# Performance work log

Hardware: AMD Instinct MI355X
Metric: run time of the kernel (lower is better)

The kernel has to match this reference:

```python
import jax, jax.numpy as jnp
import numpy as np

B, S, D = 512, 199, 128
PRO, SKILL = 20000, 500


def setup_inputs() -> dict:
    key = jax.random.key(0)
    ks = jax.random.split(key, 32)
    rn = lambda k, shape: jax.random.normal(k, shape, dtype=jnp.float32) * 0.05
    inp = {}
    inp["last_problem"] = jax.random.randint(ks[0], (B, S), 0, PRO, dtype=jnp.int32)
    inp["last_skill"] = jax.random.randint(ks[1], (B, S), 0, SKILL, dtype=jnp.int32)
    inp["last_ans"] = jax.random.randint(ks[2], (B, S), 0, 2, dtype=jnp.int32)
    inp["next_problem"] = jax.random.randint(ks[3], (B, S), 0, PRO, dtype=jnp.int32)
    inp["next_skill"] = jax.random.randint(ks[4], (B, S), 0, SKILL, dtype=jnp.int32)
    inp["next_ans"] = jax.random.randint(ks[5], (B, S), 0, 2, dtype=jnp.int32)
    inp["pro_embed"] = rn(ks[6], (PRO, D))
    inp["skill_embed"] = rn(ks[7], (SKILL, D))
    inp["ans_embed"] = rn(ks[8], (2, D))
    inp["time_embed"] = rn(ks[9], (200, D))
    inp["ls_state"] = rn(ks[10], (1, D))
    inp["pro_state0"] = rn(ks[11], (199, D))
    inp["skill_state0"] = rn(ks[12], (199, D))
    inp["akt_pro_diff"] = rn(ks[13], (PRO, 1))
    inp["akt_pro_change"] = rn(ks[14], (SKILL, D))
    # Linear weights stored as [in, out] (torch W.T); biases zero-init.
    inp["W_pf"] = rn(ks[15], (2 * D, D)); inp["b_pf"] = jnp.zeros((D,), jnp.float32)
    inp["W_sf"] = rn(ks[16], (2 * D, D)); inp["b_sf"] = jnp.zeros((D,), jnp.float32)
    inp["W_af"] = rn(ks[17], (2 * D, D)); inp["b_af"] = jnp.zeros((D,), jnp.float32)
    inp["W_ps"] = rn(ks[18], (2 * D, D)); inp["b_ps"] = jnp.zeros((D,), jnp.float32)
    inp["W_ss"] = rn(ks[19], (2 * D, D)); inp["b_ss"] = jnp.zeros((D,), jnp.float32)
    inp["W_as"] = rn(ks[20], (2 * D, D)); inp["b_as"] = jnp.zeros((D,), jnp.float32)
    inp["W_o1"] = rn(ks[21], (4 * D, D)); inp["b_o1"] = jnp.zeros((D,), jnp.float32)
    inp["W_o2"] = rn(ks[22], (D, 1));     inp["b_o2"] = jnp.zeros((1,), jnp.float32)
    return inp


def _forward(next_problem, next_skill, next_ans,
             pro_embed, skill_embed, ans_embed, time_embed, ls_state,
             pro_state0, skill_state0, akt_pro_diff, akt_pro_change,
             W_pf, b_pf, W_sf, b_sf, W_af, b_af,
             W_ps, b_ps, W_ss, b_ss, W_as, b_as,
             W_o1, b_o1, W_o2, b_o2):
    Bb, Ss = next_problem.shape
    Dd = pro_embed.shape[1]
    # [B,S,D] question embedding with AKT-style difficulty modulation
    npe = (pro_embed[next_problem] + skill_embed[next_skill]
           + akt_pro_diff[next_problem] * akt_pro_change[next_skill])
    nX = npe + ans_embed[next_ans]
    atge = time_embed[1]  # all_time_gap == 1 every step
    bidx = jnp.arange(Bb)

    def step(carry, x):
        pro_state, skill_state, all_state, lpt_tab, lst_tab = carry
        t, npe_t, nX_t, pidx, sidx = x
        # gather last-seen states via per-batch time indices
        lpt = lpt_tab[bidx, pidx]               # [B] int
        lbp = pro_state[bidx, lpt]              # [B,D]
        tge = time_embed[t - lpt]               # [B,D]
        lst = lst_tab[bidx, sidx]
        lbs = skill_state[bidx, lst]
        stge = time_embed[t - lst]
        # forget gates
        lbp = lbp * jax.nn.sigmoid(jnp.concatenate([lbp, tge], -1) @ W_pf + b_pf)
        lbs = lbs * jax.nn.sigmoid(jnp.concatenate([lbs, stge], -1) @ W_sf + b_sf)
        atge_b = jnp.broadcast_to(atge, all_state.shape)
        la = all_state * jax.nn.sigmoid(jnp.concatenate([all_state, atge_b], -1) @ W_af + b_af)
        # prediction head
        final = jnp.concatenate([la, lbp, lbs, npe_t], -1)  # [B,4D]
        P = jax.nn.sigmoid(jax.nn.relu(final @ W_o1 + b_o1) @ W_o2 + b_o2)[:, 0]
        # state updates
        new_all = la + jnp.tanh(jnp.concatenate([la, nX_t], -1) @ W_as + b_as)
        new_pro = lbp + jnp.tanh(jnp.concatenate([lbp, nX_t], -1) @ W_ps + b_ps)
        new_skill = lbs + jnp.tanh(jnp.concatenate([lbs, nX_t], -1) @ W_ss + b_ss)
        # scatter time and state back
        lpt_tab = lpt_tab.at[bidx, pidx].set(t)
        lst_tab = lst_tab.at[bidx, sidx].set(t)
        pro_state = jax.lax.dynamic_update_slice_in_dim(pro_state, new_pro[:, None, :], t, axis=1)
        skill_state = jax.lax.dynamic_update_slice_in_dim(skill_state, new_skill[:, None, :], t, axis=1)
        return (pro_state, skill_state, new_all, lpt_tab, lst_tab), P

    init = (jnp.broadcast_to(pro_state0[None], (Bb, pro_state0.shape[0], Dd)),
            jnp.broadcast_to(skill_state0[None], (Bb, skill_state0.shape[0], Dd)),
            jnp.broadcast_to(ls_state, (Bb, Dd)),
            jnp.zeros((Bb, akt_pro_diff.shape[0]), jnp.int32),
            jnp.zeros((Bb, akt_pro_change.shape[0]), jnp.int32))
    xs = (jnp.arange(Ss, dtype=jnp.int32),
          jnp.swapaxes(npe, 0, 1), jnp.swapaxes(nX, 0, 1),
          next_problem.T, next_skill.T)
    _, Ps = jax.lax.scan(step, init, xs)  # Ps: [S,B]
    return Ps.T  # [B,S]


def reference(last_problem, last_skill, last_ans, next_problem, next_skill, next_ans,
              pro_embed, skill_embed, ans_embed, time_embed, ls_state,
              pro_state0, skill_state0, akt_pro_diff, akt_pro_change,
              W_pf, b_pf, W_sf, b_sf, W_af, b_af,
              W_ps, b_ps, W_ss, b_ss, W_as, b_as,
              W_o1, b_o1, W_o2, b_o2):
    # last_problem/last_skill/last_ans are only used for shape in the original forward
    return _forward(next_problem, next_skill, next_ans,
                    pro_embed, skill_embed, ans_embed, time_embed, ls_state,
                    pro_state0, skill_state0, akt_pro_diff, akt_pro_change,
                    W_pf, b_pf, W_sf, b_sf, W_af, b_af,
                    W_ps, b_ps, W_ss, b_ss, W_as, b_as,
                    W_o1, b_o1, W_o2, b_o2)
```

## Files before the change

kernel.cpp:

```cpp
#include <hip/hip_runtime.h>
#include <hip/hip_bf16.h>

typedef __bf16 bf16;
typedef bf16 bf16x8 __attribute__((ext_vector_type(8)));
typedef bf16 bf16x4 __attribute__((ext_vector_type(4)));
typedef float f32x4 __attribute__((ext_vector_type(4)));
typedef unsigned short u16;

#define Bsz 512
#define Ssz 199
#define Dsz 128
#define GR 16
#define NBLK (Bsz / GR)
#define BTot (Bsz * Ssz)

__device__ __forceinline__ float sigmoidf_(float x) { return 1.f / (1.f + __expf(-x)); }
__device__ __forceinline__ float tanhf_(float x) {
  float xc = fminf(fmaxf(x, -15.f), 15.f);
  float e = __expf(2.f * xc);
  return (e - 1.f) / (e + 1.f);
}
__device__ __forceinline__ f32x4 mfma16(bf16x8 a, bf16x8 b, f32x4 c) {
  return __builtin_amdgcn_mfma_f32_16x16x32_bf16(a, b, c, 0, 0, 0);
}
__device__ __forceinline__ bf16x8 ldfrag(const bf16* PW, int KS, int nt, int ks, int lane) {
  return *(const bf16x8*)&PW[(size_t)((nt * KS + ks) * 64 + lane) * 8];
}

__global__ void k_lastseen(const int* __restrict__ np_, const int* __restrict__ ns_,
                           int* __restrict__ lpt, int* __restrict__ lst) {
  __shared__ unsigned short tabP[20000];
  __shared__ unsigned short tabS[500];
  __shared__ int pbuf[Ssz], sbuf[Ssz];
  int b = blockIdx.x;
  for (int i = threadIdx.x; i < 20000; i += blockDim.x) tabP[i] = 0;
  for (int i = threadIdx.x; i < 500; i += blockDim.x) tabS[i] = 0;
  for (int i = threadIdx.x; i < Ssz; i += blockDim.x) {
    pbuf[i] = np_[b * Ssz + i];
    sbuf[i] = ns_[b * Ssz + i];
  }
  __syncthreads();
  if (threadIdx.x == 0) {
    for (int t = 0; t < Ssz; ++t) {
      int p = pbuf[t], s = sbuf[t];
      lpt[b * Ssz + t] = tabP[p]; tabP[p] = (unsigned short)t;
      lst[b * Ssz + t] = tabS[s]; tabS[s] = (unsigned short)t;
    }
  }
}

__global__ void k_pack(const float* __restrict__ W, bf16* __restrict__ dst, int K) {
  int g = blockIdx.x * blockDim.x + threadIdx.x;
  int KS = K / 32;
  int total = 8 * KS * 64;
  if (g >= total) return;
  int l = g & 63;
  int ks = (g >> 6) % KS;
  int nt = (g >> 6) / KS;
  int col = nt * 16 + (l & 15);
  int k0 = ks * 32 + (l >> 4) * 8;
  bf16x8 v;
  for (int j = 0; j < 8; ++j) v[j] = (bf16)W[(size_t)(k0 + j) * 128 + col];
  *(bf16x8*)&dst[(size_t)g * 8] = v;
}

__global__ void k_tge(const float* __restrict__ TE, const float* __restrict__ W,
                      const float* __restrict__ bias, float* __restrict__ dst) {
  __shared__ float te[128];
  int d = blockIdx.x, n = threadIdx.x;
  te[n] = TE[d * 128 + n];
  __syncthreads();
  float acc = bias[n];
  for (int k = 0; k < 128; ++k) acc += te[k] * W[(size_t)(128 + k) * 128 + n];
  dst[d * 128 + n] = acc;
}

struct MainParams {
  const int *next_problem, *next_skill, *next_ans;
  const float *pro_embed, *skill_embed, *ans_embed;
  const float *akt_pro_diff, *akt_pro_change;
  const float *ls_state, *pro_state0, *skill_state0;
  const int *lpt, *lst;
  const float *TGEp, *TGEs, *cAF;
  const bf16 *PWpf, *PWsf, *PWaf, *PWps, *PWss, *PWas, *PWo1;
  const float *b_ps, *b_ss, *b_as, *b_o1, *W_o2, *b_o2;
  bf16 *proSt, *skSt;
  bf16 *Sla, *Slbp, *Slbs;
  float *out;
};

template <int IH>
__global__ void __launch_bounds__(512, 2) k_main(MainParams P) {
  const int b0 = blockIdx.x * GR;
  const int tid = threadIdx.x;
  const int lane = tid & 63;
  const int wv = tid >> 6;
  const int r32 = tid >> 5;
  const int c4 = (tid & 31) * 4;
  const int arow = lane & 15, apos = (lane >> 4) * 8;
  const int rb = (lane >> 4) * 4;
  const int cA = wv * 16 + (lane & 15);

  __shared__ __align__(16) bf16 Ala[16][136], Albp[16][136], Albs[16][136], AnX[16][136];
  __shared__ __align__(16) bf16 Anpe[IH ? 16 : 1][136];
  __shared__ __align__(16) float GPp[16][128], GPs[16][128];
  __shared__ __align__(16) bf16 STG[2][16][128];
  __shared__ float Hh[IH ? 16 : 1][132];
  __shared__ float Hpart[IH ? 16 : 1][16];
  __shared__ float w2s[IH ? 128 : 1];
  __shared__ u16 lptL[GR * Ssz], lstL[GR * Ssz], npL[GR * Ssz], nsnaL[GR * Ssz];

  bf16x8 Wpf[4], Wsf[4], Waf[4], Wps[8], Wss[8], Was[8];
#pragma unroll
  for (int ks = 0; ks < 4; ++ks) {
    Wpf[ks] = ldfrag(P.PWpf, 4, wv, ks, lane);
    Wsf[ks] = ldfrag(P.PWsf, 4, wv, ks, lane);
    Waf[ks] = ldfrag(P.PWaf, 4, wv, ks, lane);
  }
#pragma unroll
  for (int ks = 0; ks < 8; ++ks) {
    Wps[ks] = ldfrag(P.PWps, 8, wv, ks, lane);
    Wss[ks] = ldfrag(P.PWss, 8, wv, ks, lane);
    Was[ks] = ldfrag(P.PWas, 8, wv, ks, lane);
  }
  const float bpsv = P.b_ps[cA], bssv = P.b_ss[cA], basv = P.b_as[cA], cafv = P.cAF[cA];
  float bo1v = 0.f, bo2 = 0.f;
  if (IH) {
    bo1v = P.b_o1[cA];
    bo2 = P.b_o2[0];
    if (tid < 128) w2s[tid] = P.W_o2[tid];
  }

  for (int i = tid; i < GR * Ssz; i += 512) {
    int r = i / Ssz, tt = i - r * Ssz;
    int bt = (b0 + r) * Ssz + tt;
    lptL[i] = (u16)P.lpt[bt];
    lstL[i] = (u16)P.lst[bt];
    npL[i] = (u16)P.next_problem[bt];
    nsnaL[i] = (u16)((P.next_skill[bt] << 1) | P.next_ans[bt]);
  }
  __syncthreads();

  {
    bf16x4 va, vp, vs;
    for (int j = 0; j < 4; ++j) {
      va[j] = (bf16)P.ls_state[c4 + j];
      vp[j] = (bf16)P.pro_state0[c4 + j];
      vs[j] = (bf16)P.skill_state0[c4 + j];
    }
    *(bf16x4*)&Ala[r32][c4] = va;
    *(bf16x4*)&Albp[r32][c4] = vp;
    *(bf16x4*)&Albs[r32][c4] = vs;
    *(f32x4*)&GPp[r32][c4] = *(const f32x4*)&P.TGEp[c4];
    *(f32x4*)&GPs[r32][c4] = *(const f32x4*)&P.TGEs[c4];
    int ii = r32 * Ssz;
    int np = npL[ii];
    int sa = nsnaL[ii];
    int ns = sa >> 1, na = sa & 1;
    float diff = P.akt_pro_diff[np];
    f32x4 pe = *(const f32x4*)&P.pro_embed[(size_t)np * Dsz + c4];
    f32x4 se = *(const f32x4*)&P.skill_embed[(size_t)ns * Dsz + c4];
    f32x4 ch = *(const f32x4*)&P.akt_pro_change[(size_t)ns * Dsz + c4];
    f32x4 ae = *(const f32x4*)&P.ans_embed[(size_t)na * Dsz + c4];
    bf16x4 vx, vn;
    for (int j = 0; j < 4; ++j) {
      float f = pe[j] + se[j] + diff * ch[j];
      vn[j] = (bf16)f;
      vx[j] = (bf16)(f + ae[j]);
    }
    *(bf16x4*)&AnX[r32][c4] = vx;
    if (IH) *(bf16x4*)&Anpe[r32][c4] = vn;
  }
  __syncthreads();

  for (int t = 0; t < Ssz; ++t) {
    int lpN = 0, lsN = 0;
    bf16x4 pPro{}, pSk{};
    f32x4 pGp{}, pGs{}, pe{}, se{}, ch{}, ae{};
    float diff = 0.f;
    if (t + 1 < Ssz) {
      int ii = r32 * Ssz + t + 1;
      lpN = lptL[ii];
      lsN = lstL[ii];
      int np = npL[ii];
      int sa = nsnaL[ii];
      int ns = sa >> 1, na = sa & 1;
      if (lpN != t)
        pPro = *(const bf16x4*)&P.proSt[((size_t)(b0 + r32) * Ssz + lpN) * Dsz + c4];
      if (lsN != t)
        pSk = *(const bf16x4*)&P.skSt[((size_t)(b0 + r32) * Ssz + lsN) * Dsz + c4];
      pGp = *(const f32x4*)&P.TGEp[(size_t)(t + 1 - lpN) * Dsz + c4];
      pGs = *(const f32x4*)&P.TGEs[(size_t)(t + 1 - lsN) * Dsz + c4];
      diff = P.akt_pro_diff[np];
      pe = *(const f32x4*)&P.pro_embed[(size_t)np * Dsz + c4];
      se = *(const f32x4*)&P.skill_embed[(size_t)ns * Dsz + c4];
      ch = *(const f32x4*)&P.akt_pro_change[(size_t)ns * Dsz + c4];
      ae = *(const f32x4*)&P.ans_embed[(size_t)na * Dsz + c4];
    }
    if (IH && t > 0 && tid < 16) {
      float s = 0.f;
      for (int k = 0; k < 16; ++k) s += Hpart[tid][k];
      P.out[(size_t)(b0 + tid) * Ssz + (t - 1)] = sigmoidf_(s + bo2);
    }
    f32x4 dpf{}, dsf{}, daf{};
#pragma unroll
    for (int ks = 0; ks < 4; ++ks) {
      bf16x8 ap = *(const bf16x8*)&Albp[arow][ks * 32 + apos];
      bf16x8 av = *(const bf16x8*)&Albs[arow][ks * 32 + apos];
      bf16x8 aa = *(const bf16x8*)&Ala[arow][ks * 32 + apos];
      dpf = mfma16(ap, Wpf[ks], dpf);
      dsf = mfma16(av, Wsf[ks], dsf);
      daf = mfma16(aa, Waf[ks], daf);
    }
    __syncthreads();
#pragma unroll
    for (int r = 0; r < 4; ++r) {
      int row = rb + r;
      float gp = sigmoidf_(dpf[r] + GPp[row][cA]);
      Albp[row][cA] = (bf16)((float)Albp[row][cA] * gp);
      float gs = sigmoidf_(dsf[r] + GPs[row][cA]);
      Albs[row][cA] = (bf16)((float)Albs[row][cA] * gs);
      float ga = sigmoidf_(daf[r] + cafv);
      Ala[row][cA] = (bf16)((float)Ala[row][cA] * ga);
    }
    __syncthreads();
    f32x4 uas{}, ups{}, uss{}, hh{};
#pragma unroll
    for (int ks = 0; ks < 4; ++ks) {
      bf16x8 aa = *(const bf16x8*)&Ala[arow][ks * 32 + apos];
      bf16x8 ap = *(const bf16x8*)&Albp[arow][ks * 32 + apos];
      bf16x8 av = *(const bf16x8*)&Albs[arow][ks * 32 + apos];
      bf16x8 ax = *(const bf16x8*)&AnX[arow][ks * 32 + apos];
      uas = mfma16(aa, Was[ks], uas);
      uas = mfma16(ax, Was[ks + 4], uas);
      ups = mfma16(ap, Wps[ks], ups);
      ups = mfma16(ax, Wps[ks + 4], ups);
      uss = mfma16(av, Wss[ks], uss);
      uss = mfma16(ax, Wss[ks + 4], uss);
      if (IH) {
        bf16x8 an = *(const bf16x8*)&Anpe[arow][ks * 32 + apos];
        hh = mfma16(aa, ldfrag(P.PWo1, 16, wv, ks, lane), hh);
        hh = mfma16(ap, ldfrag(P.PWo1, 16, wv, ks + 4, lane), hh);
        hh = mfma16(av, ldfrag(P.PWo1, 16, wv, ks + 8, lane), hh);
        hh = mfma16(an, ldfrag(P.PWo1, 16, wv, ks + 12, lane), hh);
      }
    }
    __syncthreads();
#pragma unroll
    for (int r = 0; r < 4; ++r) {
      int row = rb + r;
      float lav = (float)Ala[row][cA];
      float lbpv = (float)Albp[row][cA];
      float lbsv = (float)Albs[row][cA];
      Ala[row][cA] = (bf16)(lav + tanhf_(uas[r] + basv));
      STG[0][row][cA] = (bf16)(lbpv + tanhf_(ups[r] + bpsv));
      STG[1][row][cA] = (bf16)(lbsv + tanhf_(uss[r] + bssv));
      if (!IH) P.Sla[((size_t)(b0 + row) * Ssz + t) * Dsz + cA] = (bf16)lav;
      if (IH) Hh[row][cA] = fmaxf(hh[r] + bo1v, 0.f);
    }
    __syncthreads();
    if (!IH) {
      *(bf16x4*)&P.Slbp[((size_t)(b0 + r32) * Ssz + t) * Dsz + c4] =
          *(const bf16x4*)&Albp[r32][c4];
      *(bf16x4*)&P.Slbs[((size_t)(b0 + r32) * Ssz + t) * Dsz + c4] =
          *(const bf16x4*)&Albs[r32][c4];
    }
    bf16x4 npv = *(const bf16x4*)&STG[0][r32][c4];
    bf16x4 nsv = *(const bf16x4*)&STG[1][r32][c4];
    *(bf16x4*)&P.proSt[((size_t)(b0 + r32) * Ssz + t) * Dsz + c4] = npv;
    *(bf16x4*)&P.skSt[((size_t)(b0 + r32) * Ssz + t) * Dsz + c4] = nsv;
    if (t + 1 < Ssz) {
      *(bf16x4*)&Albp[r32][c4] = (lpN == t) ? npv : pPro;
      *(bf16x4*)&Albs[r32][c4] = (lsN == t) ? nsv : pSk;
      *(f32x4*)&GPp[r32][c4] = pGp;
      *(f32x4*)&GPs[r32][c4] = pGs;
      bf16x4 vx, vn;
      for (int j = 0; j < 4; ++j) {
        float f = pe[j] + se[j] + diff * ch[j];
        vn[j] = (bf16)f;
        vx[j] = (bf16)(f + ae[j]);
      }
      *(bf16x4*)&AnX[r32][c4] = vx;
      if (IH) *(bf16x4*)&Anpe[r32][c4] = vn;
    }
    if (IH && tid < 256) {
      int row = tid >> 4, cg = tid & 15;
      float s = 0.f;
      for (int j = 0; j < 8; ++j) s += Hh[row][cg * 8 + j] * w2s[cg * 8 + j];
      Hpart[row][cg] = s;
    }
    __syncthreads();
  }
  if (IH && tid < 16) {
    float s = 0.f;
    for (int k = 0; k < 16; ++k) s += Hpart[tid][k];
    P.out[(size_t)(b0 + tid) * Ssz + (Ssz - 1)] = sigmoidf_(s + bo2);
  }
}

struct HeadParams {
  const bf16 *Sla, *Slbp, *Slbs, *PWo1;
  const int *next_problem, *next_skill;
  const float *pro_embed, *skill_embed, *akt_pro_diff, *akt_pro_change;
  const float *b_o1, *W_o2, *b_o2;
  float *out;
};

__global__ void k_head(HeadParams P) {
  const int bt0 = blockIdx.x * 16;
  const int tid = threadIdx.x, lane = tid & 63, wv = tid >> 6;
  const int r16 = tid >> 4, c8 = (tid & 15) * 8;
  const int arow = lane & 15, apos = (lane >> 4) * 8;
  const int rb = (lane >> 4) * 4;
  const int nt0 = wv, nt1 = wv + 4;
  const int cAh = nt0 * 16 + (lane & 15), cBh = nt1 * 16 + (lane & 15);
  __shared__ __align__(16) bf16 Af[16][520];
  __shared__ float Hh[16][132];
  __shared__ float Hpart[16][16];
  __shared__ float w2s[128];
  if (tid < 128) w2s[tid] = P.W_o2[tid];
  {
    int bt = bt0 + r16;
    *(bf16x8*)&Af[r16][c8] = *(const bf16x8*)&P.Sla[(size_t)bt * 128 + c8];
    *(bf16x8*)&Af[r16][128 + c8] = *(const bf16x8*)&P.Slbp[(size_t)bt * 128 + c8];
    *(bf16x8*)&Af[r16][256 + c8] = *(const bf16x8*)&P.Slbs[(size_t)bt * 128 + c8];
    int np = P.next_problem[bt], ns = P.next_skill[bt];
    float diff = P.akt_pro_diff[np];
    f32x4 p0 = *(const f32x4*)&P.pro_embed[(size_t)np * 128 + c8];
    f32x4 p1 = *(const f32x4*)&P.pro_embed[(size_t)np * 128 + c8 + 4];
    f32x4 s0 = *(const f32x4*)&P.skill_embed[(size_t)ns * 128 + c8];
    f32x4 s1 = *(const f32x4*)&P.skill_embed[(size_t)ns * 128 + c8 + 4];
    f32x4 c0 = *(const f32x4*)&P.akt_pro_change[(size_t)ns * 128 + c8];
    f32x4 c1 = *(const f32x4*)&P.akt_pro_change[(size_t)ns * 128 + c8 + 4];
    bf16x8 vn;
    for (int j = 0; j < 4; ++j) {
      vn[j] = (bf16)(p0[j] + s0[j] + diff * c0[j]);
      vn[j + 4] = (bf16)(p1[j] + s1[j] + diff * c1[j]);
    }
    *(bf16x8*)&Af[r16][384 + c8] = vn;
  }
  __syncthreads();
  f32x4 h0{}, h1{};
#pragma unroll
  for (int ks = 0; ks < 16; ++ks) {
    bf16x8 a = *(const bf16x8*)&Af[arow][ks * 32 + apos];
    h0 = mfma16(a, ldfrag(P.PWo1, 16, nt0, ks, lane), h0);
    h1 = mfma16(a, ldfrag(P.PWo1, 16, nt1, ks, lane), h1);
  }
  const float bo1A = P.b_o1[cAh], bo1B = P.b_o1[cBh];
  for (int r = 0; r < 4; ++r) {
    Hh[rb + r][cAh] = fmaxf(h0[r] + bo1A, 0.f);
    Hh[rb + r][cBh] = fmaxf(h1[r] + bo1B, 0.f);
  }
  __syncthreads();
  {
    int row = tid >> 4, cg = tid & 15;
    float s = 0.f;
    for (int j = 0; j < 8; ++j) s += Hh[row][cg * 8 + j] * w2s[cg * 8 + j];
    Hpart[row][cg] = s;
  }
  __syncthreads();
  if (tid < 16) {
    float s = 0.f;
    for (int k = 0; k < 16; ++k) s += Hpart[tid][k];
    P.out[bt0 + tid] = sigmoidf_(s + P.b_o2[0]);
  }
}

extern "C" void kernel_launch(void* const* d_in, const int* in_sizes, int n_in,
                              void* d_out, int out_size, void* d_ws, size_t ws_size,
                              hipStream_t stream) {
  const int* next_problem = (const int*)d_in[3];
  const int* next_skill = (const int*)d_in[4];
  const int* next_ans = (const int*)d_in[5];
  const float* pro_embed = (const float*)d_in[6];
  const float* skill_embed = (const float*)d_in[7];
  const float* ans_embed = (const float*)d_in[8];
  const float* time_embed = (const float*)d_in[9];
  const float* ls_state = (const float*)d_in[10];
  const float* pro_state0 = (const float*)d_in[11];
  const float* skill_state0 = (const float*)d_in[12];
  const float* akt_pro_diff = (const float*)d_in[13];
  const float* akt_pro_change = (const float*)d_in[14];
  const float* W_pf = (const float*)d_in[15];
  const float* b_pf = (const float*)d_in[16];
  const float* W_sf = (const float*)d_in[17];
  const float* b_sf = (const float*)d_in[18];
  const float* W_af = (const float*)d_in[19];
  const float* b_af = (const float*)d_in[20];
  const float* W_ps = (const float*)d_in[21];
  const float* b_ps = (const float*)d_in[22];
  const float* W_ss = (const float*)d_in[23];
  const float* b_ss = (const float*)d_in[24];
  const float* W_as = (const float*)d_in[25];
  const float* b_as = (const float*)d_in[26];
  const float* W_o1 = (const float*)d_in[27];
  const float* b_o1 = (const float*)d_in[28];
  const float* W_o2 = (const float*)d_in[29];
  const float* b_o2 = (const float*)d_in[30];

  char* ws = (char*)d_ws;
  size_t off = 0;
  auto alloc = [&](size_t bytes) -> void* {
    void* p = ws + off;
    off += bytes;
    off = (off + 255) & ~(size_t)255;
    return p;
  };
  bf16* proSt = (bf16*)alloc((size_t)Bsz * Ssz * Dsz * 2);
  bf16* skSt = (bf16*)alloc((size_t)Bsz * Ssz * Dsz * 2);
  int* lpt = (int*)alloc((size_t)Bsz * Ssz * 4);
  int* lst = (int*)alloc((size_t)Bsz * Ssz * 4);
  float* TGEp = (float*)alloc(200 * 128 * 4);
  float* TGEs = (float*)alloc(200 * 128 * 4);
  float* cAF = (float*)alloc(128 * 4);
  bf16* PWpf = (bf16*)alloc(128 * 128 * 2);
  bf16* PWsf = (bf16*)alloc(128 * 128 * 2);
  bf16* PWaf = (bf16*)alloc(128 * 128 * 2);
  bf16* PWps = (bf16*)alloc(256 * 128 * 2);
  bf16* PWss = (bf16*)alloc(256 * 128 * 2);
  bf16* PWas = (bf16*)alloc(256 * 128 * 2);
  bf16* PWo1 = (bf16*)alloc(512 * 128 * 2);
  size_t off_common = off;
  bf16* Sla = (bf16*)alloc((size_t)BTot * Dsz * 2);
  bf16* Slbp = (bf16*)alloc((size_t)BTot * Dsz * 2);
  bf16* Slbs = (bf16*)alloc((size_t)BTot * Dsz * 2);
  size_t off_defer = off;

  bool defer = (off_defer <= ws_size);
  if (!defer && off_common > ws_size) {
    hipMemsetAsync(d_out, 0xFF, (size_t)out_size * 4, stream);
    return;
  }

  k_lastseen<<<Bsz, 256, 0, stream>>>(next_problem, next_skill, lpt, lst);
  k_pack<<<8, 256, 0, stream>>>(W_pf, PWpf, 128);
  k_pack<<<8, 256, 0, stream>>>(W_sf, PWsf, 128);
  k_pack<<<8, 256, 0, stream>>>(W_af, PWaf, 128);
  k_pack<<<16, 256, 0, stream>>>(W_ps, PWps, 256);
  k_pack<<<16, 256, 0, stream>>>(W_ss, PWss, 256);
  k_pack<<<16, 256, 0, stream>>>(W_as, PWas, 256);
  k_pack<<<32, 256, 0, stream>>>(W_o1, PWo1, 512);
  k_tge<<<200, 128, 0, stream>>>(time_embed, W_pf, b_pf, TGEp);
  k_tge<<<200, 128, 0, stream>>>(time_embed, W_sf, b_sf, TGEs);
  k_tge<<<1, 128, 0, stream>>>(time_embed + 128, W_af, b_af, cAF);

  MainParams mp;
  mp.next_problem = next_problem; mp.next_skill = next_skill; mp.next_ans = next_ans;
  mp.pro_embed = pro_embed; mp.skill_embed = skill_embed; mp.ans_embed = ans_embed;
  mp.akt_pro_diff = akt_pro_diff; mp.akt_pro_change = akt_pro_change;
  mp.ls_state = ls_state; mp.pro_state0 = pro_state0; mp.skill_state0 = skill_state0;
  mp.lpt = lpt; mp.lst = lst;
  mp.TGEp = TGEp; mp.TGEs = TGEs; mp.cAF = cAF;
  mp.PWpf = PWpf; mp.PWsf = PWsf; mp.PWaf = PWaf;
  mp.PWps = PWps; mp.PWss = PWss; mp.PWas = PWas; mp.PWo1 = PWo1;
  mp.b_ps = b_ps; mp.b_ss = b_ss; mp.b_as = b_as; mp.b_o1 = b_o1;
  mp.W_o2 = W_o2; mp.b_o2 = b_o2;
  mp.proSt = proSt; mp.skSt = skSt;
  mp.Sla = Sla; mp.Slbp = Slbp; mp.Slbs = Slbs;
  mp.out = (float*)d_out;

  if (defer) {
    k_main<0><<<NBLK, 512, 0, stream>>>(mp);
    HeadParams hp;
    hp.Sla = Sla; hp.Slbp = Slbp; hp.Slbs = Slbs; hp.PWo1 = PWo1;
    hp.next_problem = next_problem; hp.next_skill = next_skill;
    hp.pro_embed = pro_embed; hp.skill_embed = skill_embed;
    hp.akt_pro_diff = akt_pro_diff; hp.akt_pro_change = akt_pro_change;
    hp.b_o1 = b_o1; hp.W_o2 = W_o2; hp.b_o2 = b_o2;
    hp.out = (float*)d_out;
    k_head<<<BTot / 16, 256, 0, stream>>>(hp);
  } else {
    k_main<1><<<NBLK, 512, 0, stream>>>(mp);
  }
}
```

Measured before the change: 820.6 us.

## Restructure recurrent kernel: packed indices, precomputed embeddings, fewer barriers, fast activations

Packs last-seen problem/skill times and the answer bit into a single u32 index per step. A new pre-kernel materialises the next-problem embedding in bf16, so the serial main loop and the head kernel no longer recompute it. The main loop keeps gate time-embeddings in registers instead of LDS, cuts one barrier per step by fusing the state update and global stores, and uses lightweight LDS-only barriers. Activations now use exp2 and rcp intrinsics, and the fused-head variant is dropped so the deferred head kernel always runs. The cost is extra workspace and memory traffic for the embedding buffer, and the 8-bit packed timestamps rely on the sequence length staying under 256.

```diff
diff --git a/kernel.cpp b/kernel.cpp
--- a/kernel.cpp
+++ b/kernel.cpp
@@ -5,6 +5,7 @@
 typedef bf16 bf16x8 __attribute__((ext_vector_type(8)));
 typedef bf16 bf16x4 __attribute__((ext_vector_type(4)));
 typedef float f32x4 __attribute__((ext_vector_type(4)));
+typedef unsigned int u32;
 typedef unsigned short u16;
 
 #define Bsz 512
@@ -14,11 +15,11 @@
 #define NBLK (Bsz / GR)
 #define BTot (Bsz * Ssz)
 
-__device__ __forceinline__ float sigmoidf_(float x) { return 1.f / (1.f + __expf(-x)); }
-__device__ __forceinline__ float tanhf_(float x) {
-  float xc = fminf(fmaxf(x, -15.f), 15.f);
-  float e = __expf(2.f * xc);
-  return (e - 1.f) / (e + 1.f);
+__device__ __forceinline__ float fsig(float x) {
+  return __builtin_amdgcn_rcpf(1.f + __builtin_amdgcn_exp2f(x * -1.44269504f));
+}
+__device__ __forceinline__ float ftanh(float x) {
+  return 1.f - 2.f * __builtin_amdgcn_rcpf(1.f + __builtin_amdgcn_exp2f(x * 2.88539008f));
 }
 __device__ __forceinline__ f32x4 mfma16(bf16x8 a, bf16x8 b, f32x4 c) {
   return __builtin_amdgcn_mfma_f32_16x16x32_bf16(a, b, c, 0, 0, 0);
@@ -26,25 +27,34 @@
 __device__ __forceinline__ bf16x8 ldfrag(const bf16* PW, int KS, int nt, int ks, int lane) {
   return *(const bf16x8*)&PW[(size_t)((nt * KS + ks) * 64 + lane) * 8];
 }
-
-__global__ void k_lastseen(const int* __restrict__ np_, const int* __restrict__ ns_,
-                           int* __restrict__ lpt, int* __restrict__ lst) {
-  __shared__ unsigned short tabP[20000];
-  __shared__ unsigned short tabS[500];
-  __shared__ int pbuf[Ssz], sbuf[Ssz];
+__device__ __forceinline__ void barL() {
+  __builtin_amdgcn_sched_barrier(0);
+  asm volatile("s_waitcnt lgkmcnt(0)" ::: "memory");
+  __builtin_amdgcn_s_barrier();
+  __builtin_amdgcn_sched_barrier(0);
+}
+
+__global__ void k_idx(const int* __restrict__ np_, const int* __restrict__ ns_,
+                      const int* __restrict__ na_, u32* __restrict__ idx) {
+  __shared__ u16 tabP[20000];
+  __shared__ u16 tabS[500];
+  __shared__ u16 pb[Ssz], sb[Ssz];
+  __shared__ unsigned char ab[Ssz];
   int b = blockIdx.x;
   for (int i = threadIdx.x; i < 20000; i += blockDim.x) tabP[i] = 0;
   for (int i = threadIdx.x; i < 500; i += blockDim.x) tabS[i] = 0;
   for (int i = threadIdx.x; i < Ssz; i += blockDim.x) {
-    pbuf[i] = np_[b * Ssz + i];
-    sbuf[i] = ns_[b * Ssz + i];
+    pb[i] = (u16)np_[b * Ssz + i];
+    sb[i] = (u16)ns_[b * Ssz + i];
+    ab[i] = (unsigned char)na_[b * Ssz + i];
   }
   __syncthreads();
   if (threadIdx.x == 0) {
     for (int t = 0; t < Ssz; ++t) {
-      int p = pbuf[t], s = sbuf[t];
-      lpt[b * Ssz + t] = tabP[p]; tabP[p] = (unsigned short)t;
-      lst[b * Ssz + t] = tabS[s]; tabS[s] = (unsigned short)t;
+      int p = pb[t], s = sb[t];
+      idx[b * Ssz + t] = (u32)tabP[p] | ((u32)tabS[s] << 8) | ((u32)ab[t] << 16);
+      tabP[p] = (u16)t;
+      tabS[s] = (u16)t;
     }
   }
 }
@@ -75,22 +85,39 @@
   dst[d * 128 + n] = acc;
 }
 
+__global__ void k_embed(const int* __restrict__ np_, const int* __restrict__ ns_,
+                        const float* __restrict__ pe, const float* __restrict__ se,
+                        const float* __restrict__ diff, const float* __restrict__ chg,
+                        bf16* __restrict__ npe) {
+  int g = blockIdx.x * 256 + threadIdx.x;
+  int bt = g >> 5, cg = (g & 31) * 4;
+  if (bt >= BTot) return;
+  int p = np_[bt], s = ns_[bt];
+  float d = diff[p];
+  f32x4 a = *(const f32x4*)&pe[(size_t)p * 128 + cg];
+  f32x4 b = *(const f32x4*)&se[(size_t)s * 128 + cg];
+  f32x4 c = *(const f32x4*)&chg[(size_t)s * 128 + cg];
+  bf16x4 v;
+  for (int j = 0; j < 4; ++j) v[j] = (bf16)(a[j] + b[j] + d * c[j]);
+  *(bf16x4*)&npe[(size_t)bt * 128 + cg] = v;
+}
+
 struct MainParams {
-  const int *next_problem, *next_skill, *next_ans;
-  const float *pro_embed, *skill_embed, *ans_embed;
-  const float *akt_pro_diff, *akt_pro_change;
+  const int *next_problem, *next_skill;
+  const float *pro_embed, *skill_embed, *akt_pro_diff, *akt_pro_change;
+  const float *ans_embed;
   const float *ls_state, *pro_state0, *skill_state0;
-  const int *lpt, *lst;
+  const u32 *idx;
+  const bf16 *npe;
   const float *TGEp, *TGEs, *cAF;
-  const bf16 *PWpf, *PWsf, *PWaf, *PWps, *PWss, *PWas, *PWo1;
-  const float *b_ps, *b_ss, *b_as, *b_o1, *W_o2, *b_o2;
-  bf16 *proSt, *skSt;
-  bf16 *Sla, *Slbp, *Slbs;
-  float *out;
+  const bf16 *PWpf, *PWsf, *PWaf, *PWps, *PWss, *PWas;
+  const float *b_ps, *b_ss, *b_as;
+  bf16 *proSt, *skSt, *Sla, *Slbp, *Slbs;
 };
 
-template <int IH>
-__global__ void __launch_bounds__(512, 2) k_main(MainParams P) {
+template <int EMB>
+__global__ void __launch_bounds__(512) __attribute__((amdgpu_waves_per_eu(2, 2)))
+k_main(MainParams P) {
   const int b0 = blockIdx.x * GR;
   const int tid = threadIdx.x;
   const int lane = tid & 63;
@@ -102,13 +129,8 @@
   const int cA = wv * 16 + (lane & 15);
 
   __shared__ __align__(16) bf16 Ala[16][136], Albp[16][136], Albs[16][136], AnX[16][136];
-  __shared__ __align__(16) bf16 Anpe[IH ? 16 : 1][136];
-  __shared__ __align__(16) float GPp[16][128], GPs[16][128];
-  __shared__ __align__(16) bf16 STG[2][16][128];
-  __shared__ float Hh[IH ? 16 : 1][132];
-  __shared__ float Hpart[IH ? 16 : 1][16];
-  __shared__ float w2s[IH ? 128 : 1];
-  __shared__ u16 lptL[GR * Ssz], lstL[GR * Ssz], npL[GR * Ssz], nsnaL[GR * Ssz];
+  __shared__ __align__(16) bf16 STG0[16][132], STG1[16][132], STGa[16][132];
+  __shared__ u32 idxL[GR * Ssz];
 
   bf16x8 Wpf[4], Wsf[4], Waf[4], Wps[8], Wss[8], Was[8];
 #pragma unroll
@@ -124,23 +146,17 @@
     Was[ks] = ldfrag(P.PWas, 8, wv, ks, lane);
   }
   const float bpsv = P.b_ps[cA], bssv = P.b_ss[cA], basv = P.b_as[cA], cafv = P.cAF[cA];
-  float bo1v = 0.f, bo2 = 0.f;
-  if (IH) {
-    bo1v = P.b_o1[cA];
-    bo2 = P.b_o2[0];
-    if (tid < 128) w2s[tid] = P.W_o2[tid];
-  }
-
-  for (int i = tid; i < GR * Ssz; i += 512) {
-    int r = i / Ssz, tt = i - r * Ssz;
-    int bt = (b0 + r) * Ssz + tt;
-    lptL[i] = (u16)P.lpt[bt];
-    lstL[i] = (u16)P.lst[bt];
-    npL[i] = (u16)P.next_problem[bt];
-    nsnaL[i] = (u16)((P.next_skill[bt] << 1) | P.next_ans[bt]);
-  }
-  __syncthreads();
-
+  float aeL[4], aeH[4];
+#pragma unroll
+  for (int j = 0; j < 4; ++j) {
+    aeL[j] = P.ans_embed[c4 + j];
+    aeH[j] = P.ans_embed[128 + c4 + j];
+  }
+
+  for (int i = tid; i < GR * Ssz; i += 512) idxL[i] = P.idx[b0 * Ssz + i];
+  __syncthreads();
+
+  float gpc[4], gsc[4];
   {
     bf16x4 va, vp, vs;
     for (int j = 0; j < 4; ++j) {
@@ -151,56 +167,63 @@
     *(bf16x4*)&Ala[r32][c4] = va;
     *(bf16x4*)&Albp[r32][c4] = vp;
     *(bf16x4*)&Albs[r32][c4] = vs;
-    *(f32x4*)&GPp[r32][c4] = *(const f32x4*)&P.TGEp[c4];
-    *(f32x4*)&GPs[r32][c4] = *(const f32x4*)&P.TGEs[c4];
-    int ii = r32 * Ssz;
-    int np = npL[ii];
-    int sa = nsnaL[ii];
-    int ns = sa >> 1, na = sa & 1;
-    float diff = P.akt_pro_diff[np];
-    f32x4 pe = *(const f32x4*)&P.pro_embed[(size_t)np * Dsz + c4];
-    f32x4 se = *(const f32x4*)&P.skill_embed[(size_t)ns * Dsz + c4];
-    f32x4 ch = *(const f32x4*)&P.akt_pro_change[(size_t)ns * Dsz + c4];
-    f32x4 ae = *(const f32x4*)&P.ans_embed[(size_t)na * Dsz + c4];
-    bf16x4 vx, vn;
-    for (int j = 0; j < 4; ++j) {
-      float f = pe[j] + se[j] + diff * ch[j];
-      vn[j] = (bf16)f;
-      vx[j] = (bf16)(f + ae[j]);
-    }
+    u32 iw0 = idxL[r32 * Ssz];
+    int na0 = (iw0 >> 16) & 1;
+    f32x4 np0;
+    if (EMB) {
+      bf16x4 nb = *(const bf16x4*)&P.npe[((size_t)(b0 + r32) * Ssz) * Dsz + c4];
+      for (int j = 0; j < 4; ++j) np0[j] = (float)nb[j];
+    } else {
+      int bt = (b0 + r32) * Ssz;
+      int np = P.next_problem[bt], ns = P.next_skill[bt];
+      float d = P.akt_pro_diff[np];
+      f32x4 a = *(const f32x4*)&P.pro_embed[(size_t)np * 128 + c4];
+      f32x4 b = *(const f32x4*)&P.skill_embed[(size_t)ns * 128 + c4];
+      f32x4 c = *(const f32x4*)&P.akt_pro_change[(size_t)ns * 128 + c4];
+      for (int j = 0; j < 4; ++j) np0[j] = a[j] + b[j] + d * c[j];
+    }
+    bf16x4 vx;
+    for (int j = 0; j < 4; ++j) vx[j] = (bf16)(np0[j] + (na0 ? aeH[j] : aeL[j]));
     *(bf16x4*)&AnX[r32][c4] = vx;
-    if (IH) *(bf16x4*)&Anpe[r32][c4] = vn;
+#pragma unroll
+    for (int r = 0; r < 4; ++r) {
+      gpc[r] = P.TGEp[cA];
+      gsc[r] = P.TGEs[cA];
+    }
   }
   __syncthreads();
 
   for (int t = 0; t < Ssz; ++t) {
-    int lpN = 0, lsN = 0;
-    bf16x4 pPro{}, pSk{};
-    f32x4 pGp{}, pGs{}, pe{}, se{}, ch{}, ae{};
-    float diff = 0.f;
-    if (t + 1 < Ssz) {
-      int ii = r32 * Ssz + t + 1;
-      lpN = lptL[ii];
-      lsN = lstL[ii];
-      int np = npL[ii];
-      int sa = nsnaL[ii];
-      int ns = sa >> 1, na = sa & 1;
+    const bool pf = (t + 1 < Ssz);
+    float gpn[4], gsn[4];
+    bf16x4 pPro{}, pSk{}, pNp{};
+    f32x4 pNpF{};
+    u32 iwN = 0;
+    if (pf) {
+#pragma unroll
+      for (int r = 0; r < 4; ++r) {
+        u32 iw = idxL[(rb + r) * Ssz + t + 1];
+        int lp = iw & 255, ls = (iw >> 8) & 255;
+        gpn[r] = P.TGEp[(size_t)(t + 1 - lp) * Dsz + cA];
+        gsn[r] = P.TGEs[(size_t)(t + 1 - ls) * Dsz + cA];
+      }
+      iwN = idxL[r32 * Ssz + t + 1];
+      int lpN = iwN & 255, lsN = (iwN >> 8) & 255;
       if (lpN != t)
         pPro = *(const bf16x4*)&P.proSt[((size_t)(b0 + r32) * Ssz + lpN) * Dsz + c4];
       if (lsN != t)
         pSk = *(const bf16x4*)&P.skSt[((size_t)(b0 + r32) * Ssz + lsN) * Dsz + c4];
-      pGp = *(const f32x4*)&P.TGEp[(size_t)(t + 1 - lpN) * Dsz + c4];
-      pGs = *(const f32x4*)&P.TGEs[(size_t)(t + 1 - lsN) * Dsz + c4];
-      diff = P.akt_pro_diff[np];
-      pe = *(const f32x4*)&P.pro_embed[(size_t)np * Dsz + c4];
-      se = *(const f32x4*)&P.skill_embed[(size_t)ns * Dsz + c4];
-      ch = *(const f32x4*)&P.akt_pro_change[(size_t)ns * Dsz + c4];
-      ae = *(const f32x4*)&P.ans_embed[(size_t)na * Dsz + c4];
-    }
-    if (IH && t > 0 && tid < 16) {
-      float s = 0.f;
-      for (int k = 0; k < 16; ++k) s += Hpart[tid][k];
-      P.out[(size_t)(b0 + tid) * Ssz + (t - 1)] = sigmoidf_(s + bo2);
+      if (EMB) {
+        pNp = *(const bf16x4*)&P.npe[((size_t)(b0 + r32) * Ssz + t + 1) * Dsz + c4];
+      } else {
+        int bt = (b0 + r32) * Ssz + t + 1;
+        int np = P.next_problem[bt], ns = P.next_skill[bt];
+        float d = P.akt_pro_diff[np];
+        f32x4 a = *(const f32x4*)&P.pro_embed[(size_t)np * 128 + c4];
+        f32x4 b = *(const f32x4*)&P.skill_embed[(size_t)ns * 128 + c4];
+        f32x4 c = *(const f32x4*)&P.akt_pro_change[(size_t)ns * 128 + c4];
+        for (int j = 0; j < 4; ++j) pNpF[j] = a[j] + b[j] + d * c[j];
+      }
     }
     f32x4 dpf{}, dsf{}, daf{};
 #pragma unroll
@@ -212,19 +235,26 @@
       dsf = mfma16(av, Wsf[ks], dsf);
       daf = mfma16(aa, Waf[ks], daf);
     }
-    __syncthreads();
+    barL();
+    float gP[4], gS[4], gA[4];
 #pragma unroll
     for (int r = 0; r < 4; ++r) {
       int row = rb + r;
-      float gp = sigmoidf_(dpf[r] + GPp[row][cA]);
-      Albp[row][cA] = (bf16)((float)Albp[row][cA] * gp);
-      float gs = sigmoidf_(dsf[r] + GPs[row][cA]);
-      Albs[row][cA] = (bf16)((float)Albs[row][cA] * gs);
-      float ga = sigmoidf_(daf[r] + cafv);
-      Ala[row][cA] = (bf16)((float)Ala[row][cA] * ga);
-    }
-    __syncthreads();
-    f32x4 uas{}, ups{}, uss{}, hh{};
+      float sp = (float)Albp[row][cA];
+      float gv = sp * fsig(dpf[r] + gpc[r]);
+      gP[r] = gv;
+      Albp[row][cA] = (bf16)gv;
+      float ss = (float)Albs[row][cA];
+      float gw = ss * fsig(dsf[r] + gsc[r]);
+      gS[r] = gw;
+      Albs[row][cA] = (bf16)gw;
+      float sa = (float)Ala[row][cA];
+      float gx = sa * fsig(daf[r] + cafv);
+      gA[r] = gx;
+      Ala[row][cA] = (bf16)gx;
+    }
+    barL();
+    f32x4 uas{}, ups{}, uss{};
 #pragma unroll
     for (int ks = 0; ks < 4; ++ks) {
       bf16x8 aa = *(const bf16x8*)&Ala[arow][ks * 32 + apos];
@@ -237,75 +267,55 @@
       ups = mfma16(ax, Wps[ks + 4], ups);
       uss = mfma16(av, Wss[ks], uss);
       uss = mfma16(ax, Wss[ks + 4], uss);
-      if (IH) {
-        bf16x8 an = *(const bf16x8*)&Anpe[arow][ks * 32 + apos];
-        hh = mfma16(aa, ldfrag(P.PWo1, 16, wv, ks, lane), hh);
-        hh = mfma16(ap, ldfrag(P.PWo1, 16, wv, ks + 4, lane), hh);
-        hh = mfma16(av, ldfrag(P.PWo1, 16, wv, ks + 8, lane), hh);
-        hh = mfma16(an, ldfrag(P.PWo1, 16, wv, ks + 12, lane), hh);
-      }
-    }
-    __syncthreads();
+    }
 #pragma unroll
     for (int r = 0; r < 4; ++r) {
       int row = rb + r;
-      float lav = (float)Ala[row][cA];
-      float lbpv = (float)Albp[row][cA];
-      float lbsv = (float)Albs[row][cA];
-      Ala[row][cA] = (bf16)(lav + tanhf_(uas[r] + basv));
-      STG[0][row][cA] = (bf16)(lbpv + tanhf_(ups[r] + bpsv));
-      STG[1][row][cA] = (bf16)(lbsv + tanhf_(uss[r] + bssv));
-      if (!IH) P.Sla[((size_t)(b0 + row) * Ssz + t) * Dsz + cA] = (bf16)lav;
-      if (IH) Hh[row][cA] = fmaxf(hh[r] + bo1v, 0.f);
+      STG0[row][cA] = (bf16)(gP[r] + ftanh(ups[r] + bpsv));
+      STG1[row][cA] = (bf16)(gS[r] + ftanh(uss[r] + bssv));
+      STGa[row][cA] = (bf16)(gA[r] + ftanh(uas[r] + basv));
+    }
+    barL();
+    {
+      size_t base = ((size_t)(b0 + r32) * Ssz + t) * Dsz + c4;
+      *(bf16x4*)&P.Sla[base] = *(const bf16x4*)&Ala[r32][c4];
+      *(bf16x4*)&P.Slbp[base] = *(const bf16x4*)&Albp[r32][c4];
+      *(bf16x4*)&P.Slbs[base] = *(const bf16x4*)&Albs[r32][c4];
+      bf16x4 npv = *(const bf16x4*)&STG0[r32][c4];
+      bf16x4 nsv = *(const bf16x4*)&STG1[r32][c4];
+      *(bf16x4*)&P.proSt[base] = npv;
+      *(bf16x4*)&P.skSt[base] = nsv;
+      if (pf) {
+        int lpN = iwN & 255, lsN = (iwN >> 8) & 255, naN = (iwN >> 16) & 1;
+        *(bf16x4*)&Ala[r32][c4] = *(const bf16x4*)&STGa[r32][c4];
+        *(bf16x4*)&Albp[r32][c4] = (lpN == t) ? npv : pPro;
+        *(bf16x4*)&Albs[r32][c4] = (lsN == t) ? nsv : pSk;
+        bf16x4 vx;
+        for (int j = 0; j < 4; ++j) {
+          float f = EMB ? (float)pNp[j] : pNpF[j];
+          vx[j] = (bf16)(f + (naN ? aeH[j] : aeL[j]));
+        }
+        *(bf16x4*)&AnX[r32][c4] = vx;
+#pragma unroll
+        for (int r = 0; r < 4; ++r) {
+          gpc[r] = gpn[r];
+          gsc[r] = gsn[r];
+        }
+      }
     }
     __syncthreads();
-    if (!IH) {
-      *(bf16x4*)&P.Slbp[((size_t)(b0 + r32) * Ssz + t) * Dsz + c4] =
-          *(const bf16x4*)&Albp[r32][c4];
-      *(bf16x4*)&P.Slbs[((size_t)(b0 + r32) * Ssz + t) * Dsz + c4] =
-          *(const bf16x4*)&Albs[r32][c4];
-    }
-    bf16x4 npv = *(const bf16x4*)&STG[0][r32][c4];
-    bf16x4 nsv = *(const bf16x4*)&STG[1][r32][c4];
-    *(bf16x4*)&P.proSt[((size_t)(b0 + r32) * Ssz + t) * Dsz + c4] = npv;
-    *(bf16x4*)&P.skSt[((size_t)(b0 + r32) * Ssz + t) * Dsz + c4] = nsv;
-    if (t + 1 < Ssz) {
-      *(bf16x4*)&Albp[r32][c4] = (lpN == t) ? npv : pPro;
-      *(bf16x4*)&Albs[r32][c4] = (lsN == t) ? nsv : pSk;
-      *(f32x4*)&GPp[r32][c4] = pGp;
-      *(f32x4*)&GPs[r32][c4] = pGs;
-      bf16x4 vx, vn;
-      for (int j = 0; j < 4; ++j) {
-        float f = pe[j] + se[j] + diff * ch[j];
-        vn[j] = (bf16)f;
-        vx[j] = (bf16)(f + ae[j]);
-      }
-      *(bf16x4*)&AnX[r32][c4] = vx;
-      if (IH) *(bf16x4*)&Anpe[r32][c4] = vn;
-    }
-    if (IH && tid < 256) {
-      int row = tid >> 4, cg = tid & 15;
-      float s = 0.f;
-      for (int j = 0; j < 8; ++j) s += Hh[row][cg * 8 + j] * w2s[cg * 8 + j];
-      Hpart[row][cg] = s;
-    }
-    __syncthreads();
-  }
-  if (IH && tid < 16) {
-    float s = 0.f;
-    for (int k = 0; k < 16; ++k) s += Hpart[tid][k];
-    P.out[(size_t)(b0 + tid) * Ssz + (Ssz - 1)] = sigmoidf_(s + bo2);
   }
 }
 
 struct HeadParams {
-  const bf16 *Sla, *Slbp, *Slbs, *PWo1;
+  const bf16 *Sla, *Slbp, *Slbs, *PWo1, *npe;
   const int *next_problem, *next_skill;
   const float *pro_embed, *skill_embed, *akt_pro_diff, *akt_pro_change;
   const float *b_o1, *W_o2, *b_o2;
   float *out;
 };
 
+template <int EMB>
 __global__ void k_head(HeadParams P) {
   const int bt0 = blockIdx.x * 16;
   const int tid = threadIdx.x, lane = tid & 63, wv = tid >> 6;
@@ -324,20 +334,24 @@
     *(bf16x8*)&Af[r16][c8] = *(const bf16x8*)&P.Sla[(size_t)bt * 128 + c8];
     *(bf16x8*)&Af[r16][128 + c8] = *(const bf16x8*)&P.Slbp[(size_t)bt * 128 + c8];
     *(bf16x8*)&Af[r16][256 + c8] = *(const bf16x8*)&P.Slbs[(size_t)bt * 128 + c8];
-    int np = P.next_problem[bt], ns = P.next_skill[bt];
-    float diff = P.akt_pro_diff[np];
-    f32x4 p0 = *(const f32x4*)&P.pro_embed[(size_t)np * 128 + c8];
-    f32x4 p1 = *(const f32x4*)&P.pro_embed[(size_t)np * 128 + c8 + 4];
-    f32x4 s0 = *(const f32x4*)&P.skill_embed[(size_t)ns * 128 + c8];
-    f32x4 s1 = *(const f32x4*)&P.skill_embed[(size_t)ns * 128 + c8 + 4];
-    f32x4 c0 = *(const f32x4*)&P.akt_pro_change[(size_t)ns * 128 + c8];
-    f32x4 c1 = *(const f32x4*)&P.akt_pro_change[(size_t)ns * 128 + c8 + 4];
-    bf16x8 vn;
-    for (int j = 0; j < 4; ++j) {
-      vn[j] = (bf16)(p0[j] + s0[j] + diff * c0[j]);
-      vn[j + 4] = (bf16)(p1[j] + s1[j] + diff * c1[j]);
-    }
-    *(bf16x8*)&Af[r16][384 + c8] = vn;
+    if (EMB) {
+      *(bf16x8*)&Af[r16][384 + c8] = *(const bf16x8*)&P.npe[(size_t)bt * 128 + c8];
+    } else {
+      int np = P.next_problem[bt], ns = P.next_skill[bt];
+      float diff = P.akt_pro_diff[np];
+      f32x4 p0 = *(const f32x4*)&P.pro_embed[(size_t)np * 128 + c8];
+      f32x4 p1 = *(const f32x4*)&P.pro_embed[(size_t)np * 128 + c8 + 4];
+      f32x4 s0 = *(const f32x4*)&P.skill_embed[(size_t)ns * 128 + c8];
+      f32x4 s1 = *(const f32x4*)&P.skill_embed[(size_t)ns * 128 + c8 + 4];
+      f32x4 c0 = *(const f32x4*)&P.akt_pro_change[(size_t)ns * 128 + c8];
+      f32x4 c1 = *(const f32x4*)&P.akt_pro_change[(size_t)ns * 128 + c8 + 4];
+      bf16x8 vn;
+      for (int j = 0; j < 4; ++j) {
+        vn[j] = (bf16)(p0[j] + s0[j] + diff * c0[j]);
+        vn[j + 4] = (bf16)(p1[j] + s1[j] + diff * c1[j]);
+      }
+      *(bf16x8*)&Af[r16][384 + c8] = vn;
+    }
   }
   __syncthreads();
   f32x4 h0{}, h1{};
@@ -363,7 +377,7 @@
   if (tid < 16) {
     float s = 0.f;
     for (int k = 0; k < 16; ++k) s += Hpart[tid][k];
-    P.out[bt0 + tid] = sigmoidf_(s + P.b_o2[0]);
+    P.out[bt0 + tid] = fsig(s + P.b_o2[0]);
   }
 }
 
@@ -409,8 +423,7 @@
   };
   bf16* proSt = (bf16*)alloc((size_t)Bsz * Ssz * Dsz * 2);
   bf16* skSt = (bf16*)alloc((size_t)Bsz * Ssz * Dsz * 2);
-  int* lpt = (int*)alloc((size_t)Bsz * Ssz * 4);
-  int* lst = (int*)alloc((size_t)Bsz * Ssz * 4);
+  u32* idx = (u32*)alloc((size_t)BTot * 4);
   float* TGEp = (float*)alloc(200 * 128 * 4);
   float* TGEs = (float*)alloc(200 * 128 * 4);
   float* cAF = (float*)alloc(128 * 4);
@@ -421,19 +434,20 @@
   bf16* PWss = (bf16*)alloc(256 * 128 * 2);
   bf16* PWas = (bf16*)alloc(256 * 128 * 2);
   bf16* PWo1 = (bf16*)alloc(512 * 128 * 2);
-  size_t off_common = off;
   bf16* Sla = (bf16*)alloc((size_t)BTot * Dsz * 2);
   bf16* Slbp = (bf16*)alloc((size_t)BTot * Dsz * 2);
   bf16* Slbs = (bf16*)alloc((size_t)BTot * Dsz * 2);
-  size_t off_defer = off;
-
-  bool defer = (off_defer <= ws_size);
-  if (!defer && off_common > ws_size) {
+  size_t off_base = off;
+  bf16* npe = (bf16*)alloc((size_t)BTot * Dsz * 2);
+  size_t off_emb = off;
+
+  bool emb = (off_emb <= ws_size);
+  if (!emb && off_base > ws_size) {
     hipMemsetAsync(d_out, 0xFF, (size_t)out_size * 4, stream);
     return;
   }
 
-  k_lastseen<<<Bsz, 256, 0, stream>>>(next_problem, next_skill, lpt, lst);
+  k_idx<<<Bsz, 256, 0, stream>>>(next_problem, next_skill, next_ans, idx);
   k_pack<<<8, 256, 0, stream>>>(W_pf, PWpf, 128);
   k_pack<<<8, 256, 0, stream>>>(W_sf, PWsf, 128);
   k_pack<<<8, 256, 0, stream>>>(W_af, PWaf, 128);
@@ -444,33 +458,37 @@
   k_tge<<<200, 128, 0, stream>>>(time_embed, W_pf, b_pf, TGEp);
   k_tge<<<200, 128, 0, stream>>>(time_embed, W_sf, b_sf, TGEs);
   k_tge<<<1, 128, 0, stream>>>(time_embed + 128, W_af, b_af, cAF);
+  if (emb)
+    k_embed<<<(BTot * 32 + 255) / 256, 256, 0, stream>>>(
+        next_problem, next_skill, pro_embed, skill_embed, akt_pro_diff, akt_pro_change, npe);
 
   MainParams mp;
-  mp.next_problem = next_problem; mp.next_skill = next_skill; mp.next_ans = next_ans;
-  mp.pro_embed = pro_embed; mp.skill_embed = skill_embed; mp.ans_embed = ans_embed;
+  mp.next_problem = next_problem; mp.next_skill = next_skill;
+  mp.pro_embed = pro_embed; mp.skill_embed = skill_embed;
   mp.akt_pro_diff = akt_pro_diff; mp.akt_pro_change = akt_pro_change;
+  mp.ans_embed = ans_embed;
   mp.ls_state = ls_state; mp.pro_state0 = pro_state0; mp.skill_state0 = skill_state0;
-  mp.lpt = lpt; mp.lst = lst;
+  mp.idx = idx; mp.npe = npe;
   mp.TGEp = TGEp; mp.TGEs = TGEs; mp.cAF = cAF;
   mp.PWpf = PWpf; mp.PWsf = PWsf; mp.PWaf = PWaf;
-  mp.PWps = PWps; mp.PWss = PWss; mp.PWas = PWas; mp.PWo1 = PWo1;
-  mp.b_ps = b_ps; mp.b_ss = b_ss; mp.b_as = b_as; mp.b_o1 = b_o1;
-  mp.W_o2 = W_o2; mp.b_o2 = b_o2;
+  mp.PWps = PWps; mp.PWss = PWss; mp.PWas = PWas;
+  mp.b_ps = b_ps; mp.b_ss = b_ss; mp.b_as = b_as;
   mp.proSt = proSt; mp.skSt = skSt;
   mp.Sla = Sla; mp.Slbp = Slbp; mp.Slbs = Slbs;
-  mp.out = (float*)d_out;
-
-  if (defer) {
+
+  HeadParams hp;
+  hp.Sla = Sla; hp.Slbp = Slbp; hp.Slbs = Slbs; hp.PWo1 = PWo1; hp.npe = npe;
+  hp.next_problem = next_problem; hp.next_skill = next_skill;
+  hp.pro_embed = pro_embed; hp.skill_embed = skill_embed;
+  hp.akt_pro_diff = akt_pro_diff; hp.akt_pro_change = akt_pro_change;
+  hp.b_o1 = b_o1; hp.W_o2 = W_o2; hp.b_o2 = b_o2;
+  hp.out = (float*)d_out;
+
+  if (emb) {
+    k_main<1><<<NBLK, 512, 0, stream>>>(mp);
+    k_head<1><<<BTot / 16, 256, 0, stream>>>(hp);
+  } else {
     k_main<0><<<NBLK, 512, 0, stream>>>(mp);
-    HeadParams hp;
-    hp.Sla = Sla; hp.Slbp = Slbp; hp.Slbs = Slbs; hp.PWo1 = PWo1;
-    hp.next_problem = next_problem; hp.next_skill = next_skill;
-    hp.pro_embed = pro_embed; hp.skill_embed = skill_embed;
-    hp.akt_pro_diff = akt_pro_diff; hp.akt_pro_change = akt_pro_change;
-    hp.b_o1 = b_o1; hp.W_o2 = W_o2; hp.b_o2 = b_o2;
-    hp.out = (float*)d_out;
-    k_head<<<BTot / 16, 256, 0, stream>>>(hp);
-  } else {
-    k_main<1><<<NBLK, 512, 0, stream>>>(mp);
-  }
-}
+    k_head<0><<<BTot / 16, 256, 0, stream>>>(hp);
+  }
+}
```

Result: faster. 686.7 us (-16.3%).
